# Optimization experiments

Hardware: AMD Instinct MI355X
Metric: run time of the kernel (lower is better)

The kernel has to match this reference:

```python
import jax, jax.numpy as jnp
import numpy as np

B = 1024          # number of graphs (subjects)
N1_PER = 116      # nodes per graph, branch 1 (AAL atlas)
N2_PER = 200      # nodes per graph, branch 2 (CC200 atlas)
DEG = 16          # sparsified adjacency degree
H = 32            # hidden_dim
NUM_CLASSES = 2


def _make_graph(key, b, n, deg):
    """Block-diagonal sparse adjacency in COO form, deg edges per node within its block."""
    N = b * n
    E = N * deg
    rows = jnp.repeat(jnp.arange(N, dtype=jnp.int32), deg)
    offs = jax.random.randint(jax.random.fold_in(key, 0), (E,), 0, n, dtype=jnp.int32)
    cols = (rows // n) * n + offs
    vals = jax.random.uniform(jax.random.fold_in(key, 1), (E,), dtype=jnp.float32)
    return rows, cols, vals


def setup_inputs() -> dict:
    key = jax.random.key(0)
    ks = jax.random.split(key, 20)
    rows1, cols1, vals1 = _make_graph(ks[0], B, N1_PER, DEG)
    rows2, cols2, vals2 = _make_graph(ks[1], B, N2_PER, DEG)
    x1 = jax.random.normal(ks[2], (B * N1_PER, N1_PER), dtype=jnp.float32)
    x2 = jax.random.normal(ks[3], (B * N2_PER, N2_PER), dtype=jnp.float32)
    s = 0.1
    inp = {
        "rows1": rows1, "cols1": cols1, "vals1": vals1, "x1": x1,
        "rows2": rows2, "cols2": cols2, "vals2": vals2, "x2": x2,
        # GCN branch 116
        "W1a": jax.random.normal(ks[4], (N1_PER, H), dtype=jnp.float32) * s,
        "b1a": jnp.zeros((H,), jnp.float32),
        "W1b": jax.random.normal(ks[5], (H, H), dtype=jnp.float32) * s,
        "b1b": jnp.zeros((H,), jnp.float32),
        # GCN branch 200
        "W2a": jax.random.normal(ks[6], (N2_PER, H), dtype=jnp.float32) * s,
        "b2a": jnp.zeros((H,), jnp.float32),
        "W2b": jax.random.normal(ks[7], (H, H), dtype=jnp.float32) * s,
        "b2b": jnp.zeros((H,), jnp.float32),
        # MLP head (stored as (in, out))
        "fc1_W": jax.random.normal(ks[8], (4 * H, H), dtype=jnp.float32) * s,
        "fc1_b": jnp.zeros((H,), jnp.float32),
        "fc2_W": jax.random.normal(ks[9], (H, H // 2), dtype=jnp.float32) * s,
        "fc2_b": jnp.zeros((H // 2,), jnp.float32),
        "fc3_W": jax.random.normal(ks[10], (H // 2, NUM_CLASSES), dtype=jnp.float32) * s,
        "fc3_b": jnp.zeros((NUM_CLASSES,), jnp.float32),
    }
    return inp


def _gcn(rows, cols, vals, x, W, b):
    # support = X @ W  (dense GEMM), then sparse aggregation A @ support, then bias
    support = x @ W                              # [N, H]
    msg = vals[:, None] * support[cols]          # gather + scale, [E, H]
    agg = jax.ops.segment_sum(msg, rows, num_segments=x.shape[0])  # scatter-add
    return agg + b


def _branch(rows, cols, vals, x, Wa, ba, Wb, bb, n_per):
    h = jax.nn.relu(_gcn(rows, cols, vals, x, Wa, ba))
    h = jax.nn.relu(_gcn(rows, cols, vals, h, Wb, bb))
    h = h.reshape(-1, n_per, h.shape[-1])        # [B, n, H]
    return jnp.concatenate([h.mean(axis=1), h.max(axis=1)], axis=1)  # [B, 2H]


def reference(rows1, cols1, vals1, x1, rows2, cols2, vals2, x2,
              W1a, b1a, W1b, b1b, W2a, b2a, W2b, b2b,
              fc1_W, fc1_b, fc2_W, fc2_b, fc3_W, fc3_b):
    f116 = _branch(rows1, cols1, vals1, x1, W1a, b1a, W1b, b1b, N1_PER)
    f200 = _branch(rows2, cols2, vals2, x2, W2a, b2a, W2b, b2b, N2_PER)
    x = jnp.concatenate([f116, f200], axis=1)    # [B, 4H]
    h = jax.nn.relu(x @ fc1_W + fc1_b)           # dropout is identity at inference
    h = jax.nn.relu(h @ fc2_W + fc2_b)
    logits = h @ fc3_W + fc3_b                   # [B, 2]
    return logits
```

## Files before the change

### kernel.cpp

```cpp
#include <hip/hip_runtime.h>
#include <stdint.h>

#define NB 1024
#define N1P 116
#define N2P 200
#define HD 32
#define T1 464
#define T2 800


__device__ __forceinline__ void gll16(const void* g, void* l) {
    __builtin_amdgcn_global_load_lds(
        (const __attribute__((address_space(1))) void*)g,
        (__attribute__((address_space(3))) void*)l, 16, 0, 0);
}

template <int K>
__device__ void gemm1_tile(const float* __restrict__ xg,
                           const float* __restrict__ W,
                           float* __restrict__ Sout, float* sX) {
    constexpr int KC = 16;
    constexpr int NC = (K + KC - 1) / KC;
    const int tid = threadIdx.x;
    const int lane = tid & 63;
    const int wave = tid >> 6;
    const int ris = lane >> 2;
    const int pq = lane & 3;

    float acc[32];
#pragma unroll
    for (int c = 0; c < 32; ++c) acc[c] = 0.f;

    auto issue = [&](int kc, int buf) {
        const int k0 = kc * KC;
        const int pieces = ((K - k0) < KC ? (K - k0) : KC) >> 2;
#pragma unroll
        for (int i = 0; i < 4; ++i) {
            const int s = wave * 4 + i;
            const int row = s * 16 + ris;
            const int g = pq ^ ((row >> 1) & 3);
            if (g < pieces)
                gll16(xg + (size_t)row * K + k0 + g * 4,
                      sX + buf * 4096 + s * 256);
        }
    };

    issue(0, 0);
    __syncthreads();

    const int sw = (tid >> 1) & 3;
    int buf = 0;
#pragma unroll 1
    for (int kc = 0; kc < NC; ++kc) {
        if (kc + 1 < NC) issue(kc + 1, buf ^ 1);
        const int k0 = kc * KC;
        const int kw = (K - k0) < KC ? (K - k0) : KC;
        const float* xrow = sX + buf * 4096 + tid * 16;
#pragma unroll
        for (int G = 0; G < 4; ++G) {
            if (G * 4 < kw) {
                const float4 x4 = *(const float4*)&xrow[(G ^ sw) * 4];
                const float* wb = W + (size_t)(k0 + G * 4) * 32;
#pragma unroll
                for (int kk = 0; kk < 4; ++kk) {
                    const float xs = (&x4.x)[kk];
                    const float* w = wb + kk * 32;
#pragma unroll
                    for (int c4 = 0; c4 < 8; ++c4) {
                        const float4 wv = *(const float4*)&w[c4 * 4];
                        acc[c4 * 4 + 0] += xs * wv.x;
                        acc[c4 * 4 + 1] += xs * wv.y;
                        acc[c4 * 4 + 2] += xs * wv.z;
                        acc[c4 * 4 + 3] += xs * wv.w;
                    }
                }
            }
        }
        __syncthreads();
        buf ^= 1;
    }

    float* srow = Sout + (size_t)tid * 32;
#pragma unroll
    for (int c4 = 0; c4 < 8; ++c4) {
        float4 o;
        o.x = acc[c4 * 4 + 0]; o.y = acc[c4 * 4 + 1];
        o.z = acc[c4 * 4 + 2]; o.w = acc[c4 * 4 + 3];
        *(float4*)&srow[c4 * 4] = o;
    }
}

__global__ __launch_bounds__(256, 3) void gemm1_kernel(
        const float* __restrict__ x1, const float* __restrict__ W1a,
        float* __restrict__ S1,
        const float* __restrict__ x2, const float* __restrict__ W2a,
        float* __restrict__ S2) {
    __shared__ float sX[2 * 4096];
    const int bid = blockIdx.x;
    if (bid < T1) {
        gemm1_tile<N1P>(x1 + (size_t)bid * 256 * N1P, W1a,
                        S1 + (size_t)bid * 256 * 32, sX);
    } else {
        const int t = bid - T1;
        gemm1_tile<N2P>(x2 + (size_t)t * 256 * N2P, W2a,
                        S2 + (size_t)t * 256 * 32, sX);
    }
}

template <int NP>
__device__ void graph_phase(int g, const float* __restrict__ S,
                            const int* __restrict__ cols,
                            const float* __restrict__ vals,
                            const float* __restrict__ ba,
                            const float* __restrict__ Wb,
                            const float* __restrict__ bb,
                            float* __restrict__ feats, int foff,
                            float* sSup) {
    constexpr int ST = 33;
    const int tid = threadIdx.x;
    const int h = tid & 31, sl = tid >> 5;
    const int base = g * NP;

    const float* Sg = S + (size_t)base * 32;
    constexpr int PIECES = NP * 8;
    constexpr int PSL = (PIECES + 255) / 256;
#pragma unroll
    for (int q = 0; q < PSL; ++q) {
        const int i = tid + q * 256;
        if (i < PIECES) {
            const float4 v = *(const float4*)(Sg + (size_t)i * 4);
            *(float4*)&sSup[(i >> 3) * ST + (i & 7) * 4] = v;
        }
    }
    __syncthreads();

    float acc2[32];
    if (tid < NP) {
        float h1[32];
#pragma unroll
        for (int k = 0; k < 32; ++k) h1[k] = ba[k];
        const int4* c4p = (const int4*)(cols + ((size_t)(base + tid)) * 16);
        const float4* v4p = (const float4*)(vals + ((size_t)(base + tid)) * 16);
#pragma unroll
        for (int q = 0; q < 4; ++q) {
            const int4 c = c4p[q];
            const float4 v = v4p[q];
            const float* r0 = &sSup[(c.x - base) * ST];
            const float* r1 = &sSup[(c.y - base) * ST];
            const float* r2 = &sSup[(c.z - base) * ST];
            const float* r3 = &sSup[(c.w - base) * ST];
#pragma unroll
            for (int c8 = 0; c8 < 8; ++c8) {
                const float4 s0 = *(const float4*)&r0[c8 * 4];
                const float4 s1 = *(const float4*)&r1[c8 * 4];
                const float4 s2 = *(const float4*)&r2[c8 * 4];
                const float4 s3 = *(const float4*)&r3[c8 * 4];
                h1[c8 * 4 + 0] += v.x * s0.x + v.y * s1.x + v.z * s2.x + v.w * s3.x;
                h1[c8 * 4 + 1] += v.x * s0.y + v.y * s1.y + v.z * s2.y + v.w * s3.y;
                h1[c8 * 4 + 2] += v.x * s0.z + v.y * s1.z + v.z * s2.z + v.w * s3.z;
                h1[c8 * 4 + 3] += v.x * s0.w + v.y * s1.w + v.z * s2.w + v.w * s3.w;
            }
        }
#pragma unroll
        for (int k = 0; k < 32; ++k) h1[k] = fmaxf(h1[k], 0.f);

#pragma unroll
        for (int c = 0; c < 32; ++c) acc2[c] = 0.f;
#pragma unroll
        for (int k = 0; k < 32; ++k) {
            const float xs = h1[k];
            const float* w = Wb + k * 32;
#pragma unroll
            for (int c4 = 0; c4 < 8; ++c4) {
                const float4 wv = *(const float4*)&w[c4 * 4];
                acc2[c4 * 4 + 0] += xs * wv.x;
                acc2[c4 * 4 + 1] += xs * wv.y;
                acc2[c4 * 4 + 2] += xs * wv.z;
                acc2[c4 * 4 + 3] += xs * wv.w;
            }
        }
    }
    __syncthreads();

    if (tid < NP) {
#pragma unroll
        for (int c4 = 0; c4 < 8; ++c4) {
            float4 o;
            o.x = acc2[c4 * 4 + 0]; o.y = acc2[c4 * 4 + 1];
            o.z = acc2[c4 * 4 + 2]; o.w = acc2[c4 * 4 + 3];
            *(float4*)&sSup[tid * ST + c4 * 4] = o;
        }
    }
    __syncthreads();

    const float bB = bb[h];
    float sum = 0.f, mx = -1e30f;
#pragma unroll 1
    for (int n = sl; n < NP; n += 8) {
        const int4* c4 = (const int4*)(cols + ((size_t)(base + n)) * 16);
        const float4* v4 = (const float4*)(vals + ((size_t)(base + n)) * 16);
        float a0 = 0.f, a1 = 0.f, a2 = 0.f, a3 = 0.f;
#pragma unroll
        for (int q = 0; q < 4; ++q) {
            const int4 c = c4[q];
            const float4 v = v4[q];
            a0 += v.x * sSup[(c.x - base) * ST + h];
            a1 += v.y * sSup[(c.y - base) * ST + h];
            a2 += v.z * sSup[(c.z - base) * ST + h];
            a3 += v.w * sSup[(c.w - base) * ST + h];
        }
        const float v2 = fmaxf(bB + ((a0 + a1) + (a2 + a3)), 0.f);
        sum += v2;
        mx = fmaxf(mx, v2);
    }
    __syncthreads();

    sSup[tid] = sum;
    sSup[256 + tid] = mx;
    __syncthreads();
    if (tid < 32) {
#pragma unroll
        for (int q = 1; q < 8; ++q) {
            sum += sSup[tid + 32 * q];
            mx = fmaxf(mx, sSup[256 + tid + 32 * q]);
        }
        feats[(size_t)g * 128 + foff + tid] = sum * (1.0f / NP);
        feats[(size_t)g * 128 + foff + 32 + tid] = mx;
    }
}

__global__ __launch_bounds__(256, 3) void graph_fused(
        const float* __restrict__ S1, const int* __restrict__ cols1,
        const float* __restrict__ vals1, const float* __restrict__ b1a,
        const float* __restrict__ W1b, const float* __restrict__ b1b,
        const float* __restrict__ S2, const int* __restrict__ cols2,
        const float* __restrict__ vals2, const float* __restrict__ b2a,
        const float* __restrict__ W2b, const float* __restrict__ b2b,
        float* __restrict__ feats) {
    __shared__ float sSup[N2P * 33];
    const int bid = blockIdx.x;
    const int g = bid >> 1;
    if ((bid & 1) == 0)
        graph_phase<N1P>(g, S1, cols1, vals1, b1a, W1b, b1b, feats, 0, sSup);
    else
        graph_phase<N2P>(g, S2, cols2, vals2, b2a, W2b, b2b, feats, 64, sSup);
}

template <int ST>
__device__ __forceinline__ void agg_phase_fb(int base, int NPv,
                                             const int* __restrict__ cols,
                                             const float* __restrict__ vals,
                                             const float* __restrict__ sup,
                                             float bias, float* __restrict__ outh,
                                             int tid) {
    const int h = tid & 31;
    for (int n = tid >> 5; n < NPv; n += 8) {
        const int4* c4 = (const int4*)(cols + ((size_t)base + n) * 16);
        const float4* v4 = (const float4*)(vals + ((size_t)base + n) * 16);
        float a = bias;
#pragma unroll
        for (int q = 0; q < 4; ++q) {
            const int4 c = c4[q];
            const float4 v = v4[q];
            a += v.x * sup[(c.x - base) * ST + h];
            a += v.y * sup[(c.y - base) * ST + h];
            a += v.z * sup[(c.z - base) * ST + h];
            a += v.w * sup[(c.w - base) * ST + h];
        }
        outh[n * ST + h] = fmaxf(a, 0.f);
    }
}

template <int NP>
__device__ void branch_graph(int g,
                             const float* __restrict__ X,
                             const int* __restrict__ cols,
                             const float* __restrict__ vals,
                             const float* __restrict__ Wa,
                             const float* __restrict__ ba,
                             const float* __restrict__ Wb,
                             const float* __restrict__ bb,
                             float* __restrict__ feats, int foff,
                             float* sSup, float* sH) {
    constexpr int ST = 33;
    constexpr int KC = 16;
    constexpr int SXS = 20;
    constexpr int NSLOT = NP * 4;
    constexpr int PSL = (NSLOT + 255) / 256;

    const int tid = threadIdx.x;
    const int base = g * NP;
    const float* xg = X + (size_t)base * NP;
    const float bA = ba[tid & 31];
    const float bB = bb[tid & 31];

    float* sX = sSup;

    float acc[32];
#pragma unroll
    for (int c = 0; c < 32; ++c) acc[c] = 0.f;

    const int NC = (NP + KC - 1) / KC;

    float4 cur[PSL], nxt[PSL];

    auto load_chunk = [&](int kc, float4* buf) {
        const int k0 = kc * KC;
        const int kw = (NP - k0) < KC ? (NP - k0) : KC;
        const int pieces = kw >> 2;
#pragma unroll
        for (int q = 0; q < PSL; ++q) {
            const int i = tid + q * 256;
            float4 v = make_float4(0.f, 0.f, 0.f, 0.f);
            if (i < NSLOT) {
                const int row = i >> 2, p = i & 3;
                if (p < pieces)
                    v = *(const float4*)(xg + (size_t)row * NP + k0 + p * 4);
            }
            buf[q] = v;
        }
    };
    auto store_chunk = [&](const float4* buf) {
#pragma unroll
        for (int q = 0; q < PSL; ++q) {
            const int i = tid + q * 256;
            if (i < NSLOT) {
                const int row = i >> 2, p = i & 3;
                *(float4*)&sX[row * SXS + p * 4] = buf[q];
            }
        }
    };

    load_chunk(0, cur);
#pragma unroll 1
    for (int kc = 0; kc < NC; ++kc) {
        __syncthreads();
        store_chunk(cur);
        __syncthreads();
        if (kc + 1 < NC) load_chunk(kc + 1, nxt);
        const int k0 = kc * KC;
        const int kw = (NP - k0) < KC ? (NP - k0) : KC;
        if (tid < NP) {
            const float* xrow = &sX[tid * SXS];
            const float* wb0 = Wa + (size_t)k0 * 32;
#pragma unroll 1
            for (int k4 = 0; k4 < kw; k4 += 4) {
                const float4 x4 = *(const float4*)&xrow[k4];
#pragma unroll
                for (int kk = 0; kk < 4; ++kk) {
                    const float xs = (&x4.x)[kk];
                    const float* w = wb0 + (k4 + kk) * 32;
#pragma unroll
                    for (int c4 = 0; c4 < 8; ++c4) {
                        const float4 wv = *(const float4*)&w[c4 * 4];
                        acc[c4 * 4 + 0] += xs * wv.x;
                        acc[c4 * 4 + 1] += xs * wv.y;
                        acc[c4 * 4 + 2] += xs * wv.z;
                        acc[c4 * 4 + 3] += xs * wv.w;
                    }
                }
            }
        }
#pragma unroll
        for (int q = 0; q < PSL; ++q) cur[q] = nxt[q];
    }
    __syncthreads();

    if (tid < NP) {
#pragma unroll
        for (int c4 = 0; c4 < 8; ++c4) {
            float4 o;
            o.x = acc[c4 * 4 + 0]; o.y = acc[c4 * 4 + 1];
            o.z = acc[c4 * 4 + 2]; o.w = acc[c4 * 4 + 3];
            *(float4*)&sSup[tid * ST + c4 * 4] = o;
        }
    }
    __syncthreads();

    agg_phase_fb<ST>(base, NP, cols, vals, sSup, bA, sH, tid);
    __syncthreads();

    if (tid < NP) {
        float acc2[32];
#pragma unroll
        for (int c = 0; c < 32; ++c) acc2[c] = 0.f;
        const float* xrow = &sH[tid * ST];
#pragma unroll 1
        for (int k4 = 0; k4 < 32; k4 += 4) {
            const float4 x4 = *(const float4*)&xrow[k4];
#pragma unroll
            for (int kk = 0; kk < 4; ++kk) {
                const float xs = (&x4.x)[kk];
                const float* w = Wb + (k4 + kk) * 32;
#pragma unroll
                for (int c4 = 0; c4 < 8; ++c4) {
                    const float4 wv = *(const float4*)&w[c4 * 4];
                    acc2[c4 * 4 + 0] += xs * wv.x;
                    acc2[c4 * 4 + 1] += xs * wv.y;
                    acc2[c4 * 4 + 2] += xs * wv.z;
                    acc2[c4 * 4 + 3] += xs * wv.w;
                }
            }
        }
#pragma unroll
        for (int c4 = 0; c4 < 8; ++c4) {
            float4 o;
            o.x = acc2[c4 * 4 + 0]; o.y = acc2[c4 * 4 + 1];
            o.z = acc2[c4 * 4 + 2]; o.w = acc2[c4 * 4 + 3];
            *(float4*)&sSup[tid * ST + c4 * 4] = o;
        }
    }
    __syncthreads();

    agg_phase_fb<ST>(base, NP, cols, vals, sSup, bB, sH, tid);
    __syncthreads();

    const int h = tid & 31, sl = tid >> 5;
    float sum = 0.f, mx = -1e30f;
    for (int n = sl; n < NP; n += 8) {
        const float v = sH[n * ST + h];
        sum += v;
        mx = fmaxf(mx, v);
    }
    float* sS = sSup;
    float* sM = sSup + 256;
    sS[tid] = sum;
    sM[tid] = mx;
    __syncthreads();
    if (tid < 32) {
#pragma unroll
        for (int q = 1; q < 8; ++q) {
            sum += sS[tid + 32 * q];
            mx = fmaxf(mx, sM[tid + 32 * q]);
        }
        feats[(size_t)g * 128 + foff + tid] = sum * (1.0f / NP);
        feats[(size_t)g * 128 + foff + 32 + tid] = mx;
    }
}

__global__ __launch_bounds__(256, 3) void fused_branches(
        const float* __restrict__ x1, const int* __restrict__ cols1,
        const float* __restrict__ vals1,
        const float* __restrict__ W1a, const float* __restrict__ b1a,
        const float* __restrict__ W1b, const float* __restrict__ b1b,
        const float* __restrict__ x2, const int* __restrict__ cols2,
        const float* __restrict__ vals2,
        const float* __restrict__ W2a, const float* __restrict__ b2a,
        const float* __restrict__ W2b, const float* __restrict__ b2b,
        float* __restrict__ feats) {
    __shared__ float sSup[N2P * 33];
    __shared__ float sH[N2P * 33];
    const int bid = blockIdx.x;
    if (bid < NB) {
        branch_graph<N1P>(bid, x1, cols1, vals1, W1a, b1a, W1b, b1b, feats, 0,
                          sSup, sH);
    } else {
        branch_graph<N2P>(bid - NB, x2, cols2, vals2, W2a, b2a, W2b, b2b, feats,
                          64, sSup, sH);
    }
}

__global__ __launch_bounds__(256) void mlp_head(const float* __restrict__ feats,
                                                const float* __restrict__ W1,
                                                const float* __restrict__ b1,
                                                const float* __restrict__ W2,
                                                const float* __restrict__ b2,
                                                const float* __restrict__ W3,
                                                const float* __restrict__ b3,
                                                float* __restrict__ out) {
    __shared__ float sW1[128 * 32];
    __shared__ float sW2[32 * 16];
    __shared__ float sW3[16 * 2];
    __shared__ float sB1[32], sB2[16], sB3[2];
    __shared__ float sF[8 * 128];
    __shared__ float sH1[8 * 32];
    __shared__ float sH2[8 * 16];

    const int tid = threadIdx.x;
    for (int idx = tid; idx < 128 * 32; idx += 256) sW1[idx] = W1[idx];
    for (int idx = tid; idx < 32 * 16; idx += 256) sW2[idx] = W2[idx];
    if (tid < 32) { sW3[tid] = W3[tid]; sB1[tid] = b1[tid]; }
    if (tid < 16) sB2[tid] = b2[tid];
    if (tid < 2) sB3[tid] = b3[tid];
    const long g0 = (long)blockIdx.x * 8;
    for (int idx = tid; idx < 1024; idx += 256) sF[idx] = feats[g0 * 128 + idx];
    __syncthreads();

    const int g = tid >> 5, h = tid & 31;
    float a1 = sB1[h];
#pragma unroll 4
    for (int k = 0; k < 128; ++k) a1 += sF[g * 128 + k] * sW1[k * 32 + h];
    sH1[g * 32 + h] = fmaxf(a1, 0.f);
    __syncthreads();

    if (h < 16) {
        float a2 = sB2[h];
#pragma unroll
        for (int k = 0; k < 32; ++k) a2 += sH1[g * 32 + k] * sW2[k * 16 + h];
        sH2[g * 16 + h] = fmaxf(a2, 0.f);
    }
    __syncthreads();

    if (h < 2) {
        float a3 = sB3[h];
#pragma unroll
        for (int k = 0; k < 16; ++k) a3 += sH2[g * 16 + k] * sW3[k * 2 + h];
        out[(g0 + g) * 2 + h] = a3;
    }
}

extern "C" void kernel_launch(void* const* d_in, const int* in_sizes, int n_in,
                              void* d_out, int out_size, void* d_ws, size_t ws_size,
                              hipStream_t stream) {
    const int*   cols1 = (const int*)d_in[1];
    const float* vals1 = (const float*)d_in[2];
    const float* x1    = (const float*)d_in[3];
    const int*   cols2 = (const int*)d_in[5];
    const float* vals2 = (const float*)d_in[6];
    const float* x2    = (const float*)d_in[7];
    const float* W1a = (const float*)d_in[8];
    const float* b1a = (const float*)d_in[9];
    const float* W1b = (const float*)d_in[10];
    const float* b1b = (const float*)d_in[11];
    const float* W2a = (const float*)d_in[12];
    const float* b2a = (const float*)d_in[13];
    const float* W2b = (const float*)d_in[14];
    const float* b2b = (const float*)d_in[15];
    const float* fc1_W = (const float*)d_in[16];
    const float* fc1_b = (const float*)d_in[17];
    const float* fc2_W = (const float*)d_in[18];
    const float* fc2_b = (const float*)d_in[19];
    const float* fc3_W = (const float*)d_in[20];
    const float* fc3_b = (const float*)d_in[21];
    float* out = (float*)d_out;

    float* feats = (float*)d_ws;
    const size_t FEATS_N = (size_t)NB * 128;
    const size_t S1_N = (size_t)NB * N1P * 32;
    const size_t S2_N = (size_t)NB * N2P * 32;
    const size_t need = (FEATS_N + S1_N + S2_N) * sizeof(float);

    if (ws_size >= need) {
        float* S1 = feats + FEATS_N;
        float* S2 = S1 + S1_N;
        gemm1_kernel<<<T1 + T2, 256, 0, stream>>>(x1, W1a, S1, x2, W2a, S2);
        graph_fused<<<2 * NB, 256, 0, stream>>>(
            S1, cols1, vals1, b1a, W1b, b1b,
            S2, cols2, vals2, b2a, W2b, b2b, feats);
    } else {
        fused_branches<<<2 * NB, 256, 0, stream>>>(
            x1, cols1, vals1, W1a, b1a, W1b, b1b,
            x2, cols2, vals2, W2a, b2a, W2b, b2b, feats);
    }

    mlp_head<<<NB / 8, 256, 0, stream>>>(feats, fc1_W, fc1_b, fc2_W, fc2_b,
                                         fc3_W, fc3_b, out);
}
```

Baseline: 519.4 us.

## Replace GEMM barriers with vmcnt waits and register-cache edges for layer-2 aggregation

In the first GEMM, each wave now loads only the X rows it later reads. The change drops the block-wide __syncthreads and waits on outstanding global-to-LDS loads with explicit s_waitcnt vmcnt. Loads are made unconditional, so the count stays constant. In the graph phase, each node's edge cols and vals are loaded once into registers before the LDS staging. The second-layer aggregation is redone per node with float4 LDS reads into an LDS tile, and pooling then reads that tile. This removes barriers and the repeated global edge reads, but leaves the second aggregation on only NP of 256 threads and raises register pressure.

```diff
diff --git a/kernel.cpp b/kernel.cpp
--- a/kernel.cpp
+++ b/kernel.cpp
@@ -38,21 +38,26 @@
         for (int i = 0; i < 4; ++i) {
             const int s = wave * 4 + i;
             const int row = s * 16 + ris;
-            const int g = pq ^ ((row >> 1) & 3);
-            if (g < pieces)
-                gll16(xg + (size_t)row * K + k0 + g * 4,
-                      sX + buf * 4096 + s * 256);
+            int gg = pq ^ ((row >> 1) & 3);
+            if (gg >= pieces) gg = 0;
+            gll16(xg + (size_t)row * K + k0 + gg * 4,
+                  sX + buf * 4096 + s * 256);
         }
     };
 
     issue(0, 0);
-    __syncthreads();
 
     const int sw = (tid >> 1) & 3;
     int buf = 0;
 #pragma unroll 1
     for (int kc = 0; kc < NC; ++kc) {
-        if (kc + 1 < NC) issue(kc + 1, buf ^ 1);
+        if (kc + 1 < NC) {
+            issue(kc + 1, buf ^ 1);
+            asm volatile("s_waitcnt vmcnt(4)" ::: "memory");
+        } else {
+            asm volatile("s_waitcnt vmcnt(0)" ::: "memory");
+        }
+        __builtin_amdgcn_sched_barrier(0);
         const int k0 = kc * KC;
         const int kw = (K - k0) < KC ? (K - k0) : KC;
         const float* xrow = sX + buf * 4096 + tid * 16;
@@ -76,7 +81,6 @@
                 }
             }
         }
-        __syncthreads();
         buf ^= 1;
     }
 
@@ -121,6 +125,15 @@
     const int h = tid & 31, sl = tid >> 5;
     const int base = g * NP;
 
+    int4 ec0, ec1, ec2, ec3;
+    float4 ev0, ev1, ev2, ev3;
+    if (tid < NP) {
+        const int4* c4p = (const int4*)(cols + ((size_t)(base + tid)) * 16);
+        const float4* v4p = (const float4*)(vals + ((size_t)(base + tid)) * 16);
+        ec0 = c4p[0]; ec1 = c4p[1]; ec2 = c4p[2]; ec3 = c4p[3];
+        ev0 = v4p[0]; ev1 = v4p[1]; ev2 = v4p[2]; ev3 = v4p[3];
+    }
+
     const float* Sg = S + (size_t)base * 32;
     constexpr int PIECES = NP * 8;
     constexpr int PSL = (PIECES + 255) / 256;
@@ -134,33 +147,33 @@
     }
     __syncthreads();
 
+    auto agg_step = [&](const int4& c, const float4& v, float* hx) {
+        const float* r0 = &sSup[(c.x - base) * ST];
+        const float* r1 = &sSup[(c.y - base) * ST];
+        const float* r2 = &sSup[(c.z - base) * ST];
+        const float* r3 = &sSup[(c.w - base) * ST];
+#pragma unroll
+        for (int c8 = 0; c8 < 8; ++c8) {
+            const float4 s0 = *(const float4*)&r0[c8 * 4];
+            const float4 s1 = *(const float4*)&r1[c8 * 4];
+            const float4 s2 = *(const float4*)&r2[c8 * 4];
+            const float4 s3 = *(const float4*)&r3[c8 * 4];
+            hx[c8 * 4 + 0] += v.x * s0.x + v.y * s1.x + v.z * s2.x + v.w * s3.x;
+            hx[c8 * 4 + 1] += v.x * s0.y + v.y * s1.y + v.z * s2.y + v.w * s3.y;
+            hx[c8 * 4 + 2] += v.x * s0.z + v.y * s1.z + v.z * s2.z + v.w * s3.z;
+            hx[c8 * 4 + 3] += v.x * s0.w + v.y * s1.w + v.z * s2.w + v.w * s3.w;
+        }
+    };
+
     float acc2[32];
     if (tid < NP) {
         float h1[32];
 #pragma unroll
         for (int k = 0; k < 32; ++k) h1[k] = ba[k];
-        const int4* c4p = (const int4*)(cols + ((size_t)(base + tid)) * 16);
-        const float4* v4p = (const float4*)(vals + ((size_t)(base + tid)) * 16);
-#pragma unroll
-        for (int q = 0; q < 4; ++q) {
-            const int4 c = c4p[q];
-            const float4 v = v4p[q];
-            const float* r0 = &sSup[(c.x - base) * ST];
-            const float* r1 = &sSup[(c.y - base) * ST];
-            const float* r2 = &sSup[(c.z - base) * ST];
-            const float* r3 = &sSup[(c.w - base) * ST];
-#pragma unroll
-            for (int c8 = 0; c8 < 8; ++c8) {
-                const float4 s0 = *(const float4*)&r0[c8 * 4];
-                const float4 s1 = *(const float4*)&r1[c8 * 4];
-                const float4 s2 = *(const float4*)&r2[c8 * 4];
-                const float4 s3 = *(const float4*)&r3[c8 * 4];
-                h1[c8 * 4 + 0] += v.x * s0.x + v.y * s1.x + v.z * s2.x + v.w * s3.x;
-                h1[c8 * 4 + 1] += v.x * s0.y + v.y * s1.y + v.z * s2.y + v.w * s3.y;
-                h1[c8 * 4 + 2] += v.x * s0.z + v.y * s1.z + v.z * s2.z + v.w * s3.z;
-                h1[c8 * 4 + 3] += v.x * s0.w + v.y * s1.w + v.z * s2.w + v.w * s3.w;
-            }
-        }
+        agg_step(ec0, ev0, h1);
+        agg_step(ec1, ev1, h1);
+        agg_step(ec2, ev2, h1);
+        agg_step(ec3, ev3, h1);
 #pragma unroll
         for (int k = 0; k < 32; ++k) h1[k] = fmaxf(h1[k], 0.f);
 
@@ -193,25 +206,36 @@
     }
     __syncthreads();
 
-    const float bB = bb[h];
+    float h2[32];
+    if (tid < NP) {
+#pragma unroll
+        for (int k = 0; k < 32; ++k) h2[k] = bb[k];
+        agg_step(ec0, ev0, h2);
+        agg_step(ec1, ev1, h2);
+        agg_step(ec2, ev2, h2);
+        agg_step(ec3, ev3, h2);
+#pragma unroll
+        for (int k = 0; k < 32; ++k) h2[k] = fmaxf(h2[k], 0.f);
+    }
+    __syncthreads();
+
+    if (tid < NP) {
+#pragma unroll
+        for (int c4 = 0; c4 < 8; ++c4) {
+            float4 o;
+            o.x = h2[c4 * 4 + 0]; o.y = h2[c4 * 4 + 1];
+            o.z = h2[c4 * 4 + 2]; o.w = h2[c4 * 4 + 3];
+            *(float4*)&sSup[tid * ST + c4 * 4] = o;
+        }
+    }
+    __syncthreads();
+
     float sum = 0.f, mx = -1e30f;
 #pragma unroll 1
     for (int n = sl; n < NP; n += 8) {
-        const int4* c4 = (const int4*)(cols + ((size_t)(base + n)) * 16);
-        const float4* v4 = (const float4*)(vals + ((size_t)(base + n)) * 16);
-        float a0 = 0.f, a1 = 0.f, a2 = 0.f, a3 = 0.f;
-#pragma unroll
-        for (int q = 0; q < 4; ++q) {
-            const int4 c = c4[q];
-            const float4 v = v4[q];
-            a0 += v.x * sSup[(c.x - base) * ST + h];
-            a1 += v.y * sSup[(c.y - base) * ST + h];
-            a2 += v.z * sSup[(c.z - base) * ST + h];
-            a3 += v.w * sSup[(c.w - base) * ST + h];
-        }
-        const float v2 = fmaxf(bB + ((a0 + a1) + (a2 + a3)), 0.f);
-        sum += v2;
-        mx = fmaxf(mx, v2);
+        const float v = sSup[n * ST + h];
+        sum += v;
+        mx = fmaxf(mx, v);
     }
     __syncthreads();
 
```

Result: slower. 576.9 us (+11.1%).

## Load GEMM1 input rows directly into registers instead of staging through LDS

Applied to the files above, without the earlier changes.

The first-layer X@W GEMM no longer stages input tiles into shared memory with global_load_lds and barriers. Each thread now loads its own row straight from global memory as float4s into two register buffers, prefetching the next chunk while computing the current one. This removes the LDS traffic and __syncthreads, but each thread reads a strided row, so coalescing gets worse. The extra register buffers also raise register pressure.

```diff
diff --git a/kernel.cpp b/kernel.cpp
--- a/kernel.cpp
+++ b/kernel.cpp
@@ -9,57 +9,34 @@
 #define T2 800
 
 
-__device__ __forceinline__ void gll16(const void* g, void* l) {
-    __builtin_amdgcn_global_load_lds(
-        (const __attribute__((address_space(1))) void*)g,
-        (__attribute__((address_space(3))) void*)l, 16, 0, 0);
-}
-
 template <int K>
-__device__ void gemm1_tile(const float* __restrict__ xg,
-                           const float* __restrict__ W,
-                           float* __restrict__ Sout, float* sX) {
+__device__ void gemm1_row(const float* __restrict__ xr,
+                          const float* __restrict__ W,
+                          float* __restrict__ srow) {
     constexpr int KC = 16;
     constexpr int NC = (K + KC - 1) / KC;
-    const int tid = threadIdx.x;
-    const int lane = tid & 63;
-    const int wave = tid >> 6;
-    const int ris = lane >> 2;
-    const int pq = lane & 3;
 
     float acc[32];
 #pragma unroll
     for (int c = 0; c < 32; ++c) acc[c] = 0.f;
 
-    auto issue = [&](int kc, int buf) {
+    float4 cA[4], cB[4];
+
+    auto ld = [&](int kc, float4* b) {
         const int k0 = kc * KC;
         const int pieces = ((K - k0) < KC ? (K - k0) : KC) >> 2;
 #pragma unroll
-        for (int i = 0; i < 4; ++i) {
-            const int s = wave * 4 + i;
-            const int row = s * 16 + ris;
-            const int g = pq ^ ((row >> 1) & 3);
-            if (g < pieces)
-                gll16(xg + (size_t)row * K + k0 + g * 4,
-                      sX + buf * 4096 + s * 256);
-        }
+        for (int p = 0; p < 4; ++p)
+            b[p] = (p < pieces) ? *(const float4*)(xr + k0 + p * 4)
+                                : make_float4(0.f, 0.f, 0.f, 0.f);
     };
-
-    issue(0, 0);
-    __syncthreads();
-
-    const int sw = (tid >> 1) & 3;
-    int buf = 0;
-#pragma unroll 1
-    for (int kc = 0; kc < NC; ++kc) {
-        if (kc + 1 < NC) issue(kc + 1, buf ^ 1);
+    auto comp = [&](int kc, const float4* b) {
         const int k0 = kc * KC;
         const int kw = (K - k0) < KC ? (K - k0) : KC;
-        const float* xrow = sX + buf * 4096 + tid * 16;
 #pragma unroll
         for (int G = 0; G < 4; ++G) {
             if (G * 4 < kw) {
-                const float4 x4 = *(const float4*)&xrow[(G ^ sw) * 4];
+                const float4 x4 = b[G];
                 const float* wb = W + (size_t)(k0 + G * 4) * 32;
 #pragma unroll
                 for (int kk = 0; kk < 4; ++kk) {
@@ -76,11 +53,17 @@
                 }
             }
         }
-        __syncthreads();
-        buf ^= 1;
-    }
-
-    float* srow = Sout + (size_t)tid * 32;
+    };
+
+    ld(0, cA);
+#pragma unroll 1
+    for (int kc = 0; kc < NC; kc += 2) {
+        if (kc + 1 < NC) ld(kc + 1, cB);
+        comp(kc, cA);
+        if (kc + 2 < NC) ld(kc + 2, cA);
+        if (kc + 1 < NC) comp(kc + 1, cB);
+    }
+
 #pragma unroll
     for (int c4 = 0; c4 < 8; ++c4) {
         float4 o;
@@ -95,15 +78,14 @@
         float* __restrict__ S1,
         const float* __restrict__ x2, const float* __restrict__ W2a,
         float* __restrict__ S2) {
-    __shared__ float sX[2 * 4096];
     const int bid = blockIdx.x;
+    const int tid = threadIdx.x;
     if (bid < T1) {
-        gemm1_tile<N1P>(x1 + (size_t)bid * 256 * N1P, W1a,
-                        S1 + (size_t)bid * 256 * 32, sX);
+        const size_t row = (size_t)bid * 256 + tid;
+        gemm1_row<N1P>(x1 + row * N1P, W1a, S1 + row * 32);
     } else {
-        const int t = bid - T1;
-        gemm1_tile<N2P>(x2 + (size_t)t * 256 * N2P, W2a,
-                        S2 + (size_t)t * 256 * 32, sX);
+        const size_t row = (size_t)(bid - T1) * 256 + tid;
+        gemm1_row<N2P>(x2 + row * N2P, W2a, S2 + row * 32);
     }
 }
 
```

Result: slower. 530.4 us (+2.1%).
